# Performance work log

Measured on AMD Instinct MI355X. Metric: run time of the kernel, lower is better.

The kernel has to match this reference:

```python
import jax, jax.numpy as jnp
import numpy as np

H = 16          # heads_num
D = 1024        # model_dim
HD = D // H     # per-head dim
NEG = -1e9


def setup_inputs() -> dict:
    key = jax.random.key(0)
    ks = jax.random.split(key, 12)
    B, S = 4, 1024
    inp = {
        "q": jax.random.normal(ks[0], (B, S, D), jnp.float32),
        "k": jax.random.normal(ks[1], (B, S, D), jnp.float32),
        "v": jax.random.normal(ks[2], (B, S, D), jnp.float32),
        "mask": jnp.ones((B, 1, S), jnp.int32),
    }
    s = 1.0 / np.sqrt(D)
    inp["Wq"] = jax.random.normal(ks[3], (D, D), jnp.float32) * s
    inp["bq"] = jnp.zeros((D,), jnp.float32)
    inp["Wk"] = jax.random.normal(ks[4], (D, D), jnp.float32) * s
    inp["bk"] = jnp.zeros((D,), jnp.float32)
    inp["Wv"] = jax.random.normal(ks[5], (D, D), jnp.float32) * s
    inp["bv"] = jnp.zeros((D,), jnp.float32)
    inp["Wo"] = jax.random.normal(ks[6], (D, D), jnp.float32) * s
    inp["bo"] = jnp.zeros((D,), jnp.float32)
    return inp


def _split_heads(x, B):
    # [B, S, D] -> [B, H, S, HD]
    return x.reshape(B, -1, H, HD).transpose(0, 2, 1, 3)


def reference(q, k, v, mask, Wq, bq, Wk, bk, Wv, bv, Wo, bo):
    B = q.shape[0]
    qh = _split_heads(q @ Wq.T + bq, B)  # [B,H,Sq,HD]
    kh = _split_heads(k @ Wk.T + bk, B)  # [B,H,Sk,HD]
    vh = _split_heads(v @ Wv.T + bv, B)  # [B,H,Sk,HD]
    scores = jnp.einsum("bhqd,bhkd->bhqk", qh, kh) / np.sqrt(HD)
    # mask [B,1,Sk] -> unsqueeze head dim -> [B,1,1,Sk], broadcast over q and heads
    scores = jnp.where(mask[:, None] == 0, NEG, scores)
    attn = jax.nn.softmax(scores, axis=-1)  # dropout in eval mode = identity
    ctx = jnp.einsum("bhqk,bhkd->bhqd", attn, vh)
    out = ctx.transpose(0, 2, 1, 3).reshape(B, -1, D)
    return out @ Wo.T + bo
```

## Files before the change

kernel.cpp:

```cpp
#include <hip/hip_runtime.h>
#include <hip/hip_bf16.h>
#include <math.h>

typedef __bf16 bf16;
typedef __bf16 bf16x8 __attribute__((ext_vector_type(8)));
typedef __bf16 bf16x2 __attribute__((ext_vector_type(2)));
typedef float f32x4 __attribute__((ext_vector_type(4)));
typedef float f32x16 __attribute__((ext_vector_type(16)));

#define D_MODEL 1024
#define SEQ 1024
#define BATCH 4
#define NHEAD 16
#define MTOT (BATCH*SEQ)

#define QSCALE 0.18033688011112042f
#define MASKNEG -1e9f

__global__ void cast_all(const float* __restrict__ s0, const float* __restrict__ s1,
                         const float* __restrict__ s2, const float* __restrict__ s3,
                         const float* __restrict__ s4, const float* __restrict__ s5,
                         const float* __restrict__ s6,
                         bf16* d0, bf16* d1, bf16* d2, bf16* d3, bf16* d4, bf16* d5, bf16* d6) {
    int z = blockIdx.y;
    const float* s; bf16* d; int n;
    switch (z) {
        case 0: s = s0; d = d0; n = MTOT * D_MODEL; break;
        case 1: s = s1; d = d1; n = MTOT * D_MODEL; break;
        case 2: s = s2; d = d2; n = MTOT * D_MODEL; break;
        case 3: s = s3; d = d3; n = D_MODEL * D_MODEL; break;
        case 4: s = s4; d = d4; n = D_MODEL * D_MODEL; break;
        case 5: s = s5; d = d5; n = D_MODEL * D_MODEL; break;
        default: s = s6; d = d6; n = D_MODEL * D_MODEL; break;
    }
    int idx = (blockIdx.x * blockDim.x + threadIdx.x) * 8;
    int stride = gridDim.x * blockDim.x * 8;
    for (int i = idx; i < n; i += stride) {
        const float4* p = (const float4*)(s + i);
        float4 a = p[0], b = p[1];
        bf16x8 o;
        o[0] = (bf16)a.x; o[1] = (bf16)a.y; o[2] = (bf16)a.z; o[3] = (bf16)a.w;
        o[4] = (bf16)b.x; o[5] = (bf16)b.y; o[6] = (bf16)b.z; o[7] = (bf16)b.w;
        *(bf16x8*)(d + i) = o;
    }
}

template<typename OT, int MODE>
__global__ __launch_bounds__(256, 3)
void gemm_bt(const bf16* __restrict__ A0, const bf16* __restrict__ A1, const bf16* __restrict__ A2,
             const bf16* __restrict__ W0, const bf16* __restrict__ W1, const bf16* __restrict__ W2,
             const float* __restrict__ bias0, const float* __restrict__ bias1, const float* __restrict__ bias2,
             OT* __restrict__ O0, OT* __restrict__ O1, OT* __restrict__ O2) {
    constexpr int BK = 32;
    constexpr int K = D_MODEL;
    constexpr int NT = K / BK;
    __shared__ alignas(16) bf16 As[2][128 * BK];
    __shared__ alignas(16) bf16 Bs[2][128 * BK];

    int z = (MODE == 0) ? blockIdx.z : 0;
    const bf16* A = (z == 0) ? A0 : (z == 1) ? A1 : A2;
    const bf16* W = (z == 0) ? W0 : (z == 1) ? W1 : W2;
    const float* bias = (z == 0) ? bias0 : (z == 1) ? bias1 : bias2;
    OT* Out = (z == 0) ? O0 : (z == 1) ? O1 : O2;

    int tid = threadIdx.x;
    int lane = tid & 63, w = tid >> 6;
    int l15 = lane & 15, l4 = lane >> 4;
    int m0 = blockIdx.x * 128;
    int n0 = blockIdx.y * 128;
    int wm = w >> 1, wn = w & 1;

    f32x4 acc[4][4] = {};

    int srow = lane >> 2;
    int scol = (lane & 3) * 8;

    auto stage = [&](int buf, int kt) {
#pragma unroll
        for (int i = 0; i < 2; ++i) {
            int seg = w * 2 + i;
            int row = seg * 16 + srow;
            const bf16* srcA = A + (size_t)(m0 + row) * K + kt * BK + scol;
            const bf16* srcB = W + (size_t)(n0 + row) * K + kt * BK + scol;
            __builtin_amdgcn_global_load_lds(
                (const __attribute__((address_space(1))) void*)srcA,
                (__attribute__((address_space(3))) void*)(&As[buf][seg * 512]), 16, 0, 0);
            __builtin_amdgcn_global_load_lds(
                (const __attribute__((address_space(1))) void*)srcB,
                (__attribute__((address_space(3))) void*)(&Bs[buf][seg * 512]), 16, 0, 0);
        }
    };

    stage(0, 0);
    __syncthreads();

    for (int kt = 0; kt < NT; ++kt) {
        int cur = kt & 1;
        if (kt + 1 < NT) stage(cur ^ 1, kt + 1);

        const bf16* pa = &As[cur][(wm * 64 + l15) * BK + l4 * 8];
        const bf16* pb = &Bs[cur][(wn * 64 + l15) * BK + l4 * 8];
        bf16x8 af[4], bv[4];
#pragma unroll
        for (int m = 0; m < 4; ++m) af[m] = *(const bf16x8*)(pa + m * 16 * BK);
#pragma unroll
        for (int n = 0; n < 4; ++n) bv[n] = *(const bf16x8*)(pb + n * 16 * BK);
#pragma unroll
        for (int m = 0; m < 4; ++m)
#pragma unroll
            for (int n = 0; n < 4; ++n)
                acc[m][n] = __builtin_amdgcn_mfma_f32_16x16x32_bf16(af[m], bv[n], acc[m][n], 0, 0, 0);

        __syncthreads();
    }

    float bload[4];
#pragma unroll
    for (int n = 0; n < 4; ++n) bload[n] = bias[n0 + wn * 64 + n * 16 + l15];

    if (MODE == 0 && z == 2) {
#pragma unroll
        for (int m = 0; m < 4; ++m) {
            int row = m0 + wm * 64 + m * 16 + l4 * 4;
#pragma unroll
            for (int n = 0; n < 4; ++n) {
                int col = n0 + wn * 64 + n * 16 + l15;
                float bl = bload[n];
#pragma unroll
                for (int r = 0; r < 4; ++r) {
                    float vv = acc[m][n][r] + bl;
                    int rr = row + r;
                    int bb = rr >> 10, s = rr & 1023;
                    Out[((size_t)(bb * 1024 + col)) * 1024 + s] = (OT)vv;
                }
            }
        }
    } else {
        const float sc = (MODE == 0 && z == 0) ? QSCALE : 1.0f;
#pragma unroll
        for (int m = 0; m < 4; ++m) {
            int row = m0 + wm * 64 + m * 16 + l4 * 4;
#pragma unroll
            for (int n = 0; n < 4; ++n) {
                int col = n0 + wn * 64 + n * 16 + l15;
                float bl = bload[n];
#pragma unroll
                for (int r = 0; r < 4; ++r) {
                    float vv = (acc[m][n][r] + bl) * sc;
                    Out[(size_t)(row + r) * D_MODEL + col] = (OT)vv;
                }
            }
        }
    }
}

__device__ __forceinline__ unsigned pkbf(float lo, float hi2) {
    bf16x2 t; t[0] = (bf16)lo; t[1] = (bf16)hi2;
    return __builtin_bit_cast(unsigned, t);
}

__global__ __launch_bounds__(256, 2)
void attn_fwd(const bf16* __restrict__ Qp, const bf16* __restrict__ Kp,
              const bf16* __restrict__ VT, const int* __restrict__ maskp,
              bf16* __restrict__ ctx) {
    __shared__ alignas(16) bf16 Kls[2][128 * 64];
    __shared__ alignas(16) bf16 Vls[2][64 * 128];
    __shared__ alignas(16) float madd2[SEQ];
    __shared__ int tflag[16];

    int tid = threadIdx.x;
    int lane = tid & 63, w = tid >> 6;
    int l31 = lane & 31, hi = lane >> 5;

    int fid = blockIdx.x;
    int xcd = fid & 7, idx = fid >> 3;
    int by = xcd * 8 + (idx >> 3);
    int bx = idx & 7;
    int b = by >> 4, h = by & 15;
    int q0 = bx * 128;

    {
#pragma unroll
        for (int i = 0; i < 4; ++i) {
            int pos = tid + i * 256;
            madd2[pos] = maskp[b * SEQ + pos] ? 0.f : MASKNEG;
        }
#pragma unroll
        for (int i = 0; i < 4; ++i) {
            int t = w * 4 + i;
            unsigned long long bl = __ballot(maskp[b * SEQ + t * 64 + lane] != 0);
            if (lane == 0) tflag[t] = (bl == ~0ull);
        }
    }

    bf16x8 qf[4];
    {
        const bf16* qb = Qp + ((size_t)(b * SEQ + q0 + w * 32 + l31)) * D_MODEL + h * 64 + hi * 8;
#pragma unroll
        for (int ks = 0; ks < 4; ++ks) qf[ks] = *(const bf16x8*)(qb + ks * 16);
    }

    f32x16 oacc0 = {}, oacc1 = {};
    float lsum = 0.f;

    auto stage = [&](int buf, int kt) {
        int kv0 = kt * 128;
#pragma unroll
        for (int i = 0; i < 4; ++i) {
            int row = w * 32 + i * 8 + (lane >> 3);
            int cs = ((lane & 7) ^ (row & 7)) * 8;
            const bf16* srcK = Kp + ((size_t)(b * SEQ + kv0 + row)) * D_MODEL + h * 64 + cs;
            __builtin_amdgcn_global_load_lds(
                (const __attribute__((address_space(1))) void*)srcK,
                (__attribute__((address_space(3))) void*)(&Kls[buf][(w * 32 + i * 8) * 64]), 16, 0, 0);
        }
#pragma unroll
        for (int j = 0; j < 4; ++j) {
            int row = w * 16 + j * 4 + (lane >> 4);
            int cs = ((lane & 15) ^ (row & 15)) * 8;
            const bf16* srcV = VT + ((size_t)(b * 1024 + h * 64 + row)) * SEQ + kv0 + cs;
            __builtin_amdgcn_global_load_lds(
                (const __attribute__((address_space(1))) void*)srcV,
                (__attribute__((address_space(3))) void*)(&Vls[buf][(w * 16 + j * 4) * 128]), 16, 0, 0);
        }
    };

    auto half = [&](int cur, int krb, int ksb, int flag, const float* mb) {
        f32x16 p0 = {}, p1 = {};
        __builtin_amdgcn_s_setprio(1);
#pragma unroll
        for (int ks = 0; ks < 4; ++ks) {
            int sl = ((2 * ks + hi) ^ (l31 & 7)) * 8;
            bf16x8 k0 = *(const bf16x8*)(&Kls[cur][(krb + l31) * 64 + sl]);
            bf16x8 k1 = *(const bf16x8*)(&Kls[cur][(krb + 32 + l31) * 64 + sl]);
            p0 = __builtin_amdgcn_mfma_f32_32x32x16_bf16(k0, qf[ks], p0, 0, 0, 0);
            p1 = __builtin_amdgcn_mfma_f32_32x32x16_bf16(k1, qf[ks], p1, 0, 0, 0);
        }
        __builtin_amdgcn_s_setprio(0);

        float a0 = 0.f, a1 = 0.f, a2 = 0.f, a3 = 0.f;
        if (flag) {
#pragma unroll
            for (int g = 0; g < 4; ++g) {
                float s0 = 0.f, s1 = 0.f;
#pragma unroll
                for (int c = 0; c < 4; ++c) {
                    int r = g * 4 + c;
                    float e0 = exp2f(p0[r]);
                    float e1 = exp2f(p1[r]);
                    p0[r] = e0; p1[r] = e1;
                    s0 += e0; s1 += e1;
                }
                if (g == 0) a0 = s0 + s1;
                else if (g == 1) a1 = s0 + s1;
                else if (g == 2) a2 = s0 + s1;
                else a3 = s0 + s1;
            }
        } else {
#pragma unroll
            for (int g = 0; g < 4; ++g) {
                f32x4 mk0 = *(const f32x4*)(mb + g * 8 + hi * 4);
                f32x4 mk1 = *(const f32x4*)(mb + 32 + g * 8 + hi * 4);
                float s0 = 0.f, s1 = 0.f;
#pragma unroll
                for (int c = 0; c < 4; ++c) {
                    int r = g * 4 + c;
                    float e0 = exp2f(p0[r] + mk0[c]);
                    float e1 = exp2f(p1[r] + mk1[c]);
                    p0[r] = e0; p1[r] = e1;
                    s0 += e0; s1 += e1;
                }
                if (g == 0) a0 = s0 + s1;
                else if (g == 1) a1 = s0 + s1;
                else if (g == 2) a2 = s0 + s1;
                else a3 = s0 + s1;
            }
        }
        float acc_s = (a0 + a1) + (a2 + a3);
        acc_s += __shfl_xor(acc_s, 32);
        lsum += acc_s;

        union FragU { bf16x8 v; unsigned u[4]; };
        FragU pa0, pa1, pa2, pa3;
#define PKSW(PV, RA, RB, DST)  { \
            unsigned a_ = pkbf(PV[RA], PV[(RA) + 1]); \
            unsigned b_ = pkbf(PV[RB], PV[(RB) + 1]); \
            auto rr_ = __builtin_amdgcn_permlane32_swap(a_, b_, false, false); \
            DST.u[((RA) & 3) >> 1] = rr_[0]; DST.u[(((RA) & 3) >> 1) + 2] = rr_[1]; }
        PKSW(p0, 0, 4,  pa0);
        PKSW(p0, 2, 6,  pa0);
        PKSW(p0, 8, 12, pa1);
        PKSW(p0, 10, 14, pa1);
        PKSW(p1, 0, 4,  pa2);
        PKSW(p1, 2, 6,  pa2);
        PKSW(p1, 8, 12, pa3);
        PKSW(p1, 10, 14, pa3);
#undef PKSW

        __builtin_amdgcn_s_setprio(1);
#pragma unroll
        for (int i = 0; i < 4; ++i) {
            int ks = ksb + i;
            bf16x8 pav = (i == 0) ? pa0.v : (i == 1) ? pa1.v : (i == 2) ? pa2.v : pa3.v;
            int sl = ((2 * ks + hi) ^ (l31 & 15)) * 8;
            bf16x8 v0 = *(const bf16x8*)(&Vls[cur][l31 * 128 + sl]);
            bf16x8 v1 = *(const bf16x8*)(&Vls[cur][(32 + l31) * 128 + sl]);
            oacc0 = __builtin_amdgcn_mfma_f32_32x32x16_bf16(pav, v0, oacc0, 0, 0, 0);
            oacc1 = __builtin_amdgcn_mfma_f32_32x32x16_bf16(pav, v1, oacc1, 0, 0, 0);
        }
        __builtin_amdgcn_s_setprio(0);
    };

    stage(0, 0);
    __syncthreads();

    for (int kt = 0; kt < SEQ / 128; ++kt) {
        int cur = kt & 1;
        if (kt + 1 < SEQ / 128) stage(cur ^ 1, kt + 1);

        const float* mb = &madd2[kt * 128];
        half(cur, 0,  0, tflag[2 * kt],     mb);
        half(cur, 64, 4, tflag[2 * kt + 1], mb + 64);

        __syncthreads();
    }

#pragma unroll
    for (int g = 0; g < 4; ++g) {
#pragma unroll
        for (int c = 0; c < 4; ++c) {
            int r = g * 4 + c;
            int qloc = c + g * 8 + hi * 4;
            float sden = __shfl(lsum, qloc);
            float inv = 1.0f / sden;
            int qg = q0 + w * 32 + qloc;
            size_t base = ((size_t)(b * SEQ + qg)) * D_MODEL + h * 64;
            ctx[base + l31]      = (bf16)(oacc0[r] * inv);
            ctx[base + 32 + l31] = (bf16)(oacc1[r] * inv);
        }
    }
}

extern "C" void kernel_launch(void* const* d_in, const int* in_sizes, int n_in,
                              void* d_out, int out_size, void* d_ws, size_t ws_size,
                              hipStream_t stream) {
    const float* q  = (const float*)d_in[0];
    const float* k  = (const float*)d_in[1];
    const float* v  = (const float*)d_in[2];
    const int* mask = (const int*)d_in[3];
    const float* Wq = (const float*)d_in[4];
    const float* bq = (const float*)d_in[5];
    const float* Wk = (const float*)d_in[6];
    const float* bk = (const float*)d_in[7];
    const float* Wv = (const float*)d_in[8];
    const float* bv = (const float*)d_in[9];
    const float* Wo = (const float*)d_in[10];
    const float* bo = (const float*)d_in[11];
    float* out = (float*)d_out;

    char* ws = (char*)d_ws;
    size_t szQKV = (size_t)MTOT * D_MODEL * sizeof(bf16);
    size_t szW = (size_t)D_MODEL * D_MODEL * sizeof(bf16);
    bf16* qb  = (bf16*)ws; ws += szQKV;
    bf16* kb  = (bf16*)ws; ws += szQKV;
    bf16* vb  = (bf16*)ws; ws += szQKV;
    bf16* Wqb = (bf16*)ws; ws += szW;
    bf16* Wkb = (bf16*)ws; ws += szW;
    bf16* Wvb = (bf16*)ws; ws += szW;
    bf16* Wob = (bf16*)ws; ws += szW;
    bf16* Qp  = (bf16*)ws; ws += szQKV;
    bf16* Kp  = (bf16*)ws; ws += szQKV;
    bf16* VT  = (bf16*)ws; ws += szQKV;
    bf16* ctx = (bf16*)ws; ws += szQKV;

    dim3 gc(512, 7, 1);
    cast_all<<<gc, 256, 0, stream>>>(q, k, v, Wq, Wk, Wv, Wo,
                                     qb, kb, vb, Wqb, Wkb, Wvb, Wob);

    dim3 g1(MTOT / 128, D_MODEL / 128, 3);
    gemm_bt<bf16, 0><<<g1, 256, 0, stream>>>(qb, kb, vb, Wqb, Wkb, Wvb,
                                             bq, bk, bv, Qp, Kp, VT);

    attn_fwd<<<dim3(512), 256, 0, stream>>>(Qp, Kp, VT, mask, ctx);

    dim3 g3(MTOT / 128, D_MODEL / 128, 1);
    gemm_bt<float, 1><<<g3, 256, 0, stream>>>(ctx, ctx, ctx, Wob, Wob, Wob,
                                              bo, bo, bo, out, out, out);
}
```

Measured before the change: 111.8 us.

## Load K and V fragments straight from global into registers, dropping LDS staging

The attention kernel no longer stages K and V tiles in shared memory with per-tile barriers. Each wave now loads its MFMA operand fragments for K (double-buffered in registers, prefetched one tile ahead) and V directly from global memory. This removes the LDS traffic and the block-wide syncs, but every wave now reloads the same K/V data from global/L2 instead of sharing one copy. It also raises register pressure, which could hurt occupancy under launch_bounds(256,2).

```diff
diff --git a/kernel.cpp b/kernel.cpp
--- a/kernel.cpp
+++ b/kernel.cpp
@@ -163,8 +163,6 @@
 void attn_fwd(const bf16* __restrict__ Qp, const bf16* __restrict__ Kp,
               const bf16* __restrict__ VT, const int* __restrict__ maskp,
               bf16* __restrict__ ctx) {
-    __shared__ alignas(16) bf16 Kls[2][128 * 64];
-    __shared__ alignas(16) bf16 Vls[2][64 * 128];
     __shared__ alignas(16) float madd2[SEQ];
     __shared__ int tflag[16];
 
@@ -192,6 +190,7 @@
             if (lane == 0) tflag[t] = (bl == ~0ull);
         }
     }
+    __syncthreads();
 
     bf16x8 qf[4];
     {
@@ -200,46 +199,49 @@
         for (int ks = 0; ks < 4; ++ks) qf[ks] = *(const bf16x8*)(qb + ks * 16);
     }
 
+    const bf16* kb_ = Kp + ((size_t)(b * SEQ)) * D_MODEL + h * 64 + hi * 8;
+    const bf16* vb_ = VT + ((size_t)(b * 1024 + h * 64 + l31)) * SEQ + hi * 8;
+
+    auto loadK = [&](bf16x8* dst, int kv0) {
+        const bf16* p0 = kb_ + (size_t)(kv0 + l31) * D_MODEL;
+        const bf16* p1 = kb_ + (size_t)(kv0 + 32 + l31) * D_MODEL;
+#pragma unroll
+        for (int ks = 0; ks < 4; ++ks) {
+            dst[ks]     = *(const bf16x8*)(p0 + ks * 16);
+            dst[4 + ks] = *(const bf16x8*)(p1 + ks * 16);
+        }
+    };
+    auto loadV = [&](bf16x8* dst, int kv0) {
+#pragma unroll
+        for (int ks = 0; ks < 4; ++ks) {
+            dst[ks]     = *(const bf16x8*)(vb_ + kv0 + ks * 16);
+            dst[4 + ks] = *(const bf16x8*)(vb_ + (size_t)32 * SEQ + kv0 + ks * 16);
+        }
+    };
+
     f32x16 oacc0 = {}, oacc1 = {};
     float lsum = 0.f;
 
-    auto stage = [&](int buf, int kt) {
-        int kv0 = kt * 128;
-#pragma unroll
-        for (int i = 0; i < 4; ++i) {
-            int row = w * 32 + i * 8 + (lane >> 3);
-            int cs = ((lane & 7) ^ (row & 7)) * 8;
-            const bf16* srcK = Kp + ((size_t)(b * SEQ + kv0 + row)) * D_MODEL + h * 64 + cs;
-            __builtin_amdgcn_global_load_lds(
-                (const __attribute__((address_space(1))) void*)srcK,
-                (__attribute__((address_space(3))) void*)(&Kls[buf][(w * 32 + i * 8) * 64]), 16, 0, 0);
-        }
-#pragma unroll
-        for (int j = 0; j < 4; ++j) {
-            int row = w * 16 + j * 4 + (lane >> 4);
-            int cs = ((lane & 15) ^ (row & 15)) * 8;
-            const bf16* srcV = VT + ((size_t)(b * 1024 + h * 64 + row)) * SEQ + kv0 + cs;
-            __builtin_amdgcn_global_load_lds(
-                (const __attribute__((address_space(1))) void*)srcV,
-                (__attribute__((address_space(3))) void*)(&Vls[buf][(w * 16 + j * 4) * 128]), 16, 0, 0);
-        }
-    };
-
-    auto half = [&](int cur, int krb, int ksb, int flag, const float* mb) {
+    bf16x8 kfA[8], kfB[8], vf[8];
+    loadK(kfA, 0);
+
+    auto tile = [&](const bf16x8* kf, bf16x8* kn, int kt) {
+        int kv0 = kt * 64;
+        if (kt + 1 < 16) loadK(kn, kv0 + 64);
+        loadV(vf, kv0);
+
         f32x16 p0 = {}, p1 = {};
         __builtin_amdgcn_s_setprio(1);
 #pragma unroll
         for (int ks = 0; ks < 4; ++ks) {
-            int sl = ((2 * ks + hi) ^ (l31 & 7)) * 8;
-            bf16x8 k0 = *(const bf16x8*)(&Kls[cur][(krb + l31) * 64 + sl]);
-            bf16x8 k1 = *(const bf16x8*)(&Kls[cur][(krb + 32 + l31) * 64 + sl]);
-            p0 = __builtin_amdgcn_mfma_f32_32x32x16_bf16(k0, qf[ks], p0, 0, 0, 0);
-            p1 = __builtin_amdgcn_mfma_f32_32x32x16_bf16(k1, qf[ks], p1, 0, 0, 0);
+            p0 = __builtin_amdgcn_mfma_f32_32x32x16_bf16(kf[ks],     qf[ks], p0, 0, 0, 0);
+            p1 = __builtin_amdgcn_mfma_f32_32x32x16_bf16(kf[4 + ks], qf[ks], p1, 0, 0, 0);
         }
         __builtin_amdgcn_s_setprio(0);
 
         float a0 = 0.f, a1 = 0.f, a2 = 0.f, a3 = 0.f;
-        if (flag) {
+        const float* mb = &madd2[kv0];
+        if (tflag[kt]) {
 #pragma unroll
             for (int g = 0; g < 4; ++g) {
                 float s0 = 0.f, s1 = 0.f;
@@ -300,29 +302,17 @@
         __builtin_amdgcn_s_setprio(1);
 #pragma unroll
         for (int i = 0; i < 4; ++i) {
-            int ks = ksb + i;
             bf16x8 pav = (i == 0) ? pa0.v : (i == 1) ? pa1.v : (i == 2) ? pa2.v : pa3.v;
-            int sl = ((2 * ks + hi) ^ (l31 & 15)) * 8;
-            bf16x8 v0 = *(const bf16x8*)(&Vls[cur][l31 * 128 + sl]);
-            bf16x8 v1 = *(const bf16x8*)(&Vls[cur][(32 + l31) * 128 + sl]);
-            oacc0 = __builtin_amdgcn_mfma_f32_32x32x16_bf16(pav, v0, oacc0, 0, 0, 0);
-            oacc1 = __builtin_amdgcn_mfma_f32_32x32x16_bf16(pav, v1, oacc1, 0, 0, 0);
+            oacc0 = __builtin_amdgcn_mfma_f32_32x32x16_bf16(pav, vf[i],     oacc0, 0, 0, 0);
+            oacc1 = __builtin_amdgcn_mfma_f32_32x32x16_bf16(pav, vf[4 + i], oacc1, 0, 0, 0);
         }
         __builtin_amdgcn_s_setprio(0);
     };
 
-    stage(0, 0);
-    __syncthreads();
-
-    for (int kt = 0; kt < SEQ / 128; ++kt) {
-        int cur = kt & 1;
-        if (kt + 1 < SEQ / 128) stage(cur ^ 1, kt + 1);
-
-        const float* mb = &madd2[kt * 128];
-        half(cur, 0,  0, tflag[2 * kt],     mb);
-        half(cur, 64, 4, tflag[2 * kt + 1], mb + 64);
-
-        __syncthreads();
+#pragma unroll 1
+    for (int kt2 = 0; kt2 < 8; ++kt2) {
+        tile(kfA, kfB, 2 * kt2);
+        tile(kfB, kfA, 2 * kt2 + 1);
     }
 
 #pragma unroll
```

Measured after the change: 138.3 us. +23.7%, slower.

## Split attention KV range across two wave groups and merge partial outputs

Applied to the files above, without the earlier changes.

Doubles the attention block to 512 threads: two groups of four waves each process half of the key/value sequence for the same 128 queries, using 64-row tiles, then merge unnormalized outputs and row sums through shared memory. This doubles the waves per block to improve latency hiding and MFMA utilisation. It also switches exp2f to the raw hardware exp2 builtin. The cost is a shared-memory merge at the end, extra LDS use (about 68KB) that may limit blocks per CU, and higher register pressure from the 512,4 launch bounds.

```diff
diff --git a/kernel.cpp b/kernel.cpp
--- a/kernel.cpp
+++ b/kernel.cpp
@@ -16,6 +16,7 @@
 
 #define QSCALE 0.18033688011112042f
 #define MASKNEG -1e9f
+#define EXP2(x) __builtin_amdgcn_exp2f(x)
 
 __global__ void cast_all(const float* __restrict__ s0, const float* __restrict__ s1,
                          const float* __restrict__ s2, const float* __restrict__ s3,
@@ -159,18 +160,20 @@
     return __builtin_bit_cast(unsigned, t);
 }
 
-__global__ __launch_bounds__(256, 2)
+__global__ __launch_bounds__(512, 4)
 void attn_fwd(const bf16* __restrict__ Qp, const bf16* __restrict__ Kp,
               const bf16* __restrict__ VT, const int* __restrict__ maskp,
               bf16* __restrict__ ctx) {
-    __shared__ alignas(16) bf16 Kls[2][128 * 64];
-    __shared__ alignas(16) bf16 Vls[2][64 * 128];
-    __shared__ alignas(16) float madd2[SEQ];
-    __shared__ int tflag[16];
+    __shared__ alignas(16) unsigned char smem[69760];
+    bf16* Kbuf = (bf16*)smem;
+    bf16* Vbuf = (bf16*)(smem + 32768);
+    float* madd2 = (float*)(smem + 65536);
+    int* tflag = (int*)(smem + 69632);
 
     int tid = threadIdx.x;
     int lane = tid & 63, w = tid >> 6;
     int l31 = lane & 31, hi = lane >> 5;
+    int hh = w >> 2, wl = w & 3;
 
     int fid = blockIdx.x;
     int xcd = fid & 7, idx = fid >> 3;
@@ -180,14 +183,11 @@
     int q0 = bx * 128;
 
     {
-#pragma unroll
-        for (int i = 0; i < 4; ++i) {
-            int pos = tid + i * 256;
-            madd2[pos] = maskp[b * SEQ + pos] ? 0.f : MASKNEG;
-        }
-#pragma unroll
-        for (int i = 0; i < 4; ++i) {
-            int t = w * 4 + i;
+        madd2[tid] = maskp[b * SEQ + tid] ? 0.f : MASKNEG;
+        madd2[512 + tid] = maskp[b * SEQ + 512 + tid] ? 0.f : MASKNEG;
+#pragma unroll
+        for (int i = 0; i < 2; ++i) {
+            int t = w * 2 + i;
             unsigned long long bl = __ballot(maskp[b * SEQ + t * 64 + lane] != 0);
             if (lane == 0) tflag[t] = (bl == ~0ull);
         }
@@ -195,7 +195,7 @@
 
     bf16x8 qf[4];
     {
-        const bf16* qb = Qp + ((size_t)(b * SEQ + q0 + w * 32 + l31)) * D_MODEL + h * 64 + hi * 8;
+        const bf16* qb = Qp + ((size_t)(b * SEQ + q0 + wl * 32 + l31)) * D_MODEL + h * 64 + hi * 8;
 #pragma unroll
         for (int ks = 0; ks < 4; ++ks) qf[ks] = *(const bf16x8*)(qb + ks * 16);
     }
@@ -203,51 +203,59 @@
     f32x16 oacc0 = {}, oacc1 = {};
     float lsum = 0.f;
 
-    auto stage = [&](int buf, int kt) {
-        int kv0 = kt * 128;
-#pragma unroll
-        for (int i = 0; i < 4; ++i) {
-            int row = w * 32 + i * 8 + (lane >> 3);
+    auto stage = [&](int buf, int t) {
+        int kv0 = (hh * 8 + t) * 64;
+        bf16* Kd = Kbuf + (size_t)(buf * 2 + hh) * 4096;
+        bf16* Vd = Vbuf + (size_t)(buf * 2 + hh) * 4096;
+#pragma unroll
+        for (int i = 0; i < 2; ++i) {
+            int seg = wl * 2 + i;
+            int row = seg * 8 + (lane >> 3);
             int cs = ((lane & 7) ^ (row & 7)) * 8;
             const bf16* srcK = Kp + ((size_t)(b * SEQ + kv0 + row)) * D_MODEL + h * 64 + cs;
             __builtin_amdgcn_global_load_lds(
                 (const __attribute__((address_space(1))) void*)srcK,
-                (__attribute__((address_space(3))) void*)(&Kls[buf][(w * 32 + i * 8) * 64]), 16, 0, 0);
-        }
-#pragma unroll
-        for (int j = 0; j < 4; ++j) {
-            int row = w * 16 + j * 4 + (lane >> 4);
-            int cs = ((lane & 15) ^ (row & 15)) * 8;
+                (__attribute__((address_space(3))) void*)(Kd + seg * 512), 16, 0, 0);
             const bf16* srcV = VT + ((size_t)(b * 1024 + h * 64 + row)) * SEQ + kv0 + cs;
             __builtin_amdgcn_global_load_lds(
                 (const __attribute__((address_space(1))) void*)srcV,
-                (__attribute__((address_space(3))) void*)(&Vls[buf][(w * 16 + j * 4) * 128]), 16, 0, 0);
+                (__attribute__((address_space(3))) void*)(Vd + seg * 512), 16, 0, 0);
         }
     };
 
-    auto half = [&](int cur, int krb, int ksb, int flag, const float* mb) {
+    stage(0, 0);
+    __syncthreads();
+
+    for (int t = 0; t < 8; ++t) {
+        int cur = t & 1;
+        if (t + 1 < 8) stage(cur ^ 1, t + 1);
+        int kt = hh * 8 + t;
+        const bf16* Kl = Kbuf + (size_t)(cur * 2 + hh) * 4096;
+        const bf16* Vl = Vbuf + (size_t)(cur * 2 + hh) * 4096;
+
         f32x16 p0 = {}, p1 = {};
         __builtin_amdgcn_s_setprio(1);
 #pragma unroll
         for (int ks = 0; ks < 4; ++ks) {
             int sl = ((2 * ks + hi) ^ (l31 & 7)) * 8;
-            bf16x8 k0 = *(const bf16x8*)(&Kls[cur][(krb + l31) * 64 + sl]);
-            bf16x8 k1 = *(const bf16x8*)(&Kls[cur][(krb + 32 + l31) * 64 + sl]);
+            bf16x8 k0 = *(const bf16x8*)(&Kl[l31 * 64 + sl]);
+            bf16x8 k1 = *(const bf16x8*)(&Kl[(32 + l31) * 64 + sl]);
             p0 = __builtin_amdgcn_mfma_f32_32x32x16_bf16(k0, qf[ks], p0, 0, 0, 0);
             p1 = __builtin_amdgcn_mfma_f32_32x32x16_bf16(k1, qf[ks], p1, 0, 0, 0);
         }
         __builtin_amdgcn_s_setprio(0);
 
         float a0 = 0.f, a1 = 0.f, a2 = 0.f, a3 = 0.f;
-        if (flag) {
+        const float* mb = &madd2[kt * 64];
+        if (tflag[kt]) {
 #pragma unroll
             for (int g = 0; g < 4; ++g) {
                 float s0 = 0.f, s1 = 0.f;
 #pragma unroll
                 for (int c = 0; c < 4; ++c) {
                     int r = g * 4 + c;
-                    float e0 = exp2f(p0[r]);
-                    float e1 = exp2f(p1[r]);
+                    float e0 = EXP2(p0[r]);
+                    float e1 = EXP2(p1[r]);
                     p0[r] = e0; p1[r] = e1;
                     s0 += e0; s1 += e1;
                 }
@@ -265,8 +273,8 @@
 #pragma unroll
                 for (int c = 0; c < 4; ++c) {
                     int r = g * 4 + c;
-                    float e0 = exp2f(p0[r] + mk0[c]);
-                    float e1 = exp2f(p1[r] + mk1[c]);
+                    float e0 = EXP2(p0[r] + mk0[c]);
+                    float e1 = EXP2(p1[r] + mk1[c]);
                     p0[r] = e0; p1[r] = e1;
                     s0 += e0; s1 += e1;
                 }
@@ -299,44 +307,52 @@
 
         __builtin_amdgcn_s_setprio(1);
 #pragma unroll
-        for (int i = 0; i < 4; ++i) {
-            int ks = ksb + i;
-            bf16x8 pav = (i == 0) ? pa0.v : (i == 1) ? pa1.v : (i == 2) ? pa2.v : pa3.v;
-            int sl = ((2 * ks + hi) ^ (l31 & 15)) * 8;
-            bf16x8 v0 = *(const bf16x8*)(&Vls[cur][l31 * 128 + sl]);
-            bf16x8 v1 = *(const bf16x8*)(&Vls[cur][(32 + l31) * 128 + sl]);
+        for (int ks = 0; ks < 4; ++ks) {
+            bf16x8 pav = (ks == 0) ? pa0.v : (ks == 1) ? pa1.v : (ks == 2) ? pa2.v : pa3.v;
+            int sl = ((2 * ks + hi) ^ (l31 & 7)) * 8;
+            bf16x8 v0 = *(const bf16x8*)(&Vl[l31 * 64 + sl]);
+            bf16x8 v1 = *(const bf16x8*)(&Vl[(32 + l31) * 64 + sl]);
             oacc0 = __builtin_amdgcn_mfma_f32_32x32x16_bf16(pav, v0, oacc0, 0, 0, 0);
             oacc1 = __builtin_amdgcn_mfma_f32_32x32x16_bf16(pav, v1, oacc1, 0, 0, 0);
         }
         __builtin_amdgcn_s_setprio(0);
-    };
-
-    stage(0, 0);
+
+        __syncthreads();
+    }
+
+    float* Omrg = (float*)smem;
+    float* Lmrg = (float*)(smem + 32768);
+    if (hh == 1) {
+#pragma unroll
+        for (int g = 0; g < 4; ++g) {
+#pragma unroll
+            for (int c = 0; c < 4; ++c) {
+                int r = g * 4 + c;
+                int q = c + g * 8 + hi * 4;
+                Omrg[wl * 2048 + q * 64 + l31]      = oacc0[r];
+                Omrg[wl * 2048 + q * 64 + 32 + l31] = oacc1[r];
+            }
+        }
+        if (hi == 0) Lmrg[wl * 32 + l31] = lsum;
+    }
     __syncthreads();
-
-    for (int kt = 0; kt < SEQ / 128; ++kt) {
-        int cur = kt & 1;
-        if (kt + 1 < SEQ / 128) stage(cur ^ 1, kt + 1);
-
-        const float* mb = &madd2[kt * 128];
-        half(cur, 0,  0, tflag[2 * kt],     mb);
-        half(cur, 64, 4, tflag[2 * kt + 1], mb + 64);
-
-        __syncthreads();
-    }
-
-#pragma unroll
-    for (int g = 0; g < 4; ++g) {
-#pragma unroll
-        for (int c = 0; c < 4; ++c) {
-            int r = g * 4 + c;
-            int qloc = c + g * 8 + hi * 4;
-            float sden = __shfl(lsum, qloc);
-            float inv = 1.0f / sden;
-            int qg = q0 + w * 32 + qloc;
-            size_t base = ((size_t)(b * SEQ + qg)) * D_MODEL + h * 64;
-            ctx[base + l31]      = (bf16)(oacc0[r] * inv);
-            ctx[base + 32 + l31] = (bf16)(oacc1[r] * inv);
+    if (hh == 0) {
+        float ltot = lsum + Lmrg[wl * 32 + l31];
+#pragma unroll
+        for (int g = 0; g < 4; ++g) {
+#pragma unroll
+            for (int c = 0; c < 4; ++c) {
+                int r = g * 4 + c;
+                int q = c + g * 8 + hi * 4;
+                float o0 = oacc0[r] + Omrg[wl * 2048 + q * 64 + l31];
+                float o1 = oacc1[r] + Omrg[wl * 2048 + q * 64 + 32 + l31];
+                float sden = __shfl(ltot, q);
+                float inv = 1.0f / sden;
+                int qg = q0 + wl * 32 + q;
+                size_t base = ((size_t)(b * SEQ + qg)) * D_MODEL + h * 64;
+                ctx[base + l31]      = (bf16)(o0 * inv);
+                ctx[base + 32 + l31] = (bf16)(o1 * inv);
+            }
         }
     }
 }
@@ -381,7 +397,7 @@
     gemm_bt<bf16, 0><<<g1, 256, 0, stream>>>(qb, kb, vb, Wqb, Wkb, Wvb,
                                              bq, bk, bv, Qp, Kp, VT);
 
-    attn_fwd<<<dim3(512), 256, 0, stream>>>(Qp, Kp, VT, mask, ctx);
+    attn_fwd<<<dim3(512), 512, 0, stream>>>(Qp, Kp, VT, mask, ctx);
 
     dim3 g3(MTOT / 128, D_MODEL / 128, 1);
     gemm_bt<float, 1><<<g3, 256, 0, stream>>>(ctx, ctx, ctx, Wob, Wob, Wob,
```

Result: no change. 111.9 us (+0.1%).
